# Optimization experiments

Hardware: AMD Instinct MI355X
Metric: run time of the kernel (lower is better)

Reference implementation:

```python
import jax, jax.numpy as jnp
import numpy as np

EPS = 10.0
MAX_ITER = 50
THRESH = 1e-05
N, M, D = 8192, 8192, 32


def setup_inputs() -> dict:
    key = jax.random.key(0)
    k1, k2, k3, k4 = jax.random.split(key, 4)
    x = jax.random.normal(k1, (N, D), dtype=jnp.float32)
    y = jax.random.normal(k2, (M, D), dtype=jnp.float32)
    p = jax.random.uniform(k3, (N,), dtype=jnp.float32)
    q = jax.random.uniform(k4, (M,), dtype=jnp.float32)
    p = p / jnp.sum(p)  # marginals must be probability vectors
    q = q / jnp.sum(q)
    return {"x": x, "y": y, "p": p, "q": q}


def _cost_matrix_l2(x, y):
    # ||x_i - y_j||^2 via the expansion, avoiding the [N, M, D] intermediate
    x2 = jnp.sum(x * x, axis=-1)  # [N]
    y2 = jnp.sum(y * y, axis=-1)  # [M]
    C = x2[:, None] + y2[None, :] - 2.0 * (x @ y.T)  # [N, M]
    return jnp.maximum(C, 0.0)


def reference(x, y, p, q):
    C = _cost_matrix_l2(x, y)          # [N, M]
    K = jnp.exp(-C / EPS)              # [N, M]

    def step(carry, _):
        a, b, done = carry
        a_new = p / (K @ b)            # [N]
        b_new = q / (K.T @ a_new)      # [M]
        err = jnp.linalg.norm(b_new - b)
        # emulate the early break: freeze (a, b) once err < thresh was hit
        a_out = jnp.where(done, a, a_new)
        b_out = jnp.where(done, b, b_new)
        done = jnp.logical_or(done, err < THRESH)
        return (a_out, b_out, done), None

    init = (jnp.zeros_like(p), jnp.ones_like(q), jnp.array(False))
    (a, b, _), _ = jax.lax.scan(step, init, None, length=MAX_ITER)

    T = a[:, None] * K * b[None, :]    # diag(a) @ K @ diag(b)
    w_cost = jnp.sum(T * C)
    return w_cost, T
```

## Files before the change

### kernel.cpp

```cpp
#include <hip/hip_runtime.h>
#include <hip/hip_fp16.h>


#define NN 8192
#define DDIM 32
#define EPSF 10.0f
#define LOG2E 1.44269504088896340736f
#define LN2F 0.69314718055994530942f
#define KLOG2 8.0f
#define THRESH2 1e-10f

#define OFF_KS   0ull
#define OFF_PART (67108864ull)
#define OFF_A    (OFF_PART + 8388608ull)
#define OFF_B    (OFF_A + 32768ull)
#define OFF_X2   (OFF_B + 32768ull)
#define OFF_Y2   (OFF_X2 + 32768ull)
#define OFF_ERR  (OFF_Y2 + 32768ull)
#define WS_NEEDED (OFF_ERR + 4096ull)

typedef float floatx2 __attribute__((ext_vector_type(2)));

#if __has_builtin(__builtin_amdgcn_cvt_pk_f32_fp8) && __has_builtin(__builtin_amdgcn_cvt_pk_fp8_f32)
#define HW_FP8 1
#else
#define HW_FP8 0
#include <hip/hip_fp8.h>
#endif

__device__ __forceinline__ void fp8x4_to_f32(unsigned int w, float* f) {
#if HW_FP8
    floatx2 lo = __builtin_amdgcn_cvt_pk_f32_fp8((int)w, false);
    floatx2 hi = __builtin_amdgcn_cvt_pk_f32_fp8((int)w, true);
    f[0] = lo.x; f[1] = lo.y; f[2] = hi.x; f[3] = hi.y;
#else
    for (int i = 0; i < 4; ++i) {
        __hip_fp8_e4m3 h; h.__x = (__hip_fp8_storage_t)((w >> (8 * i)) & 0xff);
        f[i] = (float)h;
    }
#endif
}

__device__ __forceinline__ unsigned char f32_to_fp8(float v) {
#if HW_FP8
    return (unsigned char)(__builtin_amdgcn_cvt_pk_fp8_f32(v, v, 0, false) & 0xff);
#else
    __hip_fp8_e4m3 h(v);
    return (unsigned char)h.__x;
#endif
}

__global__ __launch_bounds__(256) void k_init(const float* __restrict__ x,
                                              const float* __restrict__ y,
                                              float* __restrict__ x2,
                                              float* __restrict__ y2,
                                              float* __restrict__ b,
                                              float* __restrict__ errpart,
                                              float* __restrict__ out) {
    int t = blockIdx.x * 256 + threadIdx.x;
    const float4* x4 = (const float4*)(x + (size_t)t * DDIM);
    float s = 0.f;
#pragma unroll
    for (int k = 0; k < 8; ++k) { float4 v = x4[k]; s += v.x*v.x + v.y*v.y + v.z*v.z + v.w*v.w; }
    x2[t] = s;
    const float4* y4 = (const float4*)(y + (size_t)t * DDIM);
    s = 0.f;
#pragma unroll
    for (int k = 0; k < 8; ++k) { float4 v = y4[k]; s += v.x*v.x + v.y*v.y + v.z*v.z + v.w*v.w; }
    y2[t] = s;
    b[t] = 1.0f;
    if (t < 256) errpart[t] = 1e30f;
    if (t == 0) out[0] = 0.f;
}

__global__ __launch_bounds__(256) void k_build(const float* __restrict__ x,
                                               const float* __restrict__ y,
                                               const float* __restrict__ x2,
                                               const float* __restrict__ y2,
                                               unsigned char* __restrict__ Ks) {
    __shared__ float yT[DDIM][256];
    __shared__ float xT[DDIM][32];
    __shared__ __align__(16) unsigned char hb8[32][256];
    const int t = threadIdx.x;
    const int jb = blockIdx.x & 31;
    const int ib = blockIdx.x >> 5;
    const int colbase = jb * 256, rowbase = ib * 32;

    {
        const float4* yp = (const float4*)(y + (size_t)(colbase + t) * DDIM);
#pragma unroll
        for (int k = 0; k < 8; ++k) {
            float4 v = yp[k];
            yT[4*k+0][t] = v.x; yT[4*k+1][t] = v.y; yT[4*k+2][t] = v.z; yT[4*k+3][t] = v.w;
        }
    }
    {
        int r = t >> 3, ds = (t & 7) * 4;
        float4 v = *(const float4*)(x + (size_t)(rowbase + r) * DDIM + ds);
        xT[ds+0][r] = v.x; xT[ds+1][r] = v.y; xT[ds+2][r] = v.z; xT[ds+3][r] = v.w;
    }
    __syncthreads();

    float acc[32];
#pragma unroll
    for (int r = 0; r < 32; ++r) acc[r] = 0.f;
    for (int d = 0; d < DDIM; ++d) {
        float yv = yT[d][t];
#pragma unroll
        for (int r4 = 0; r4 < 8; ++r4) {
            float4 xv = *(const float4*)&xT[d][r4 * 4];
            acc[r4*4+0] = fmaf(xv.x, yv, acc[r4*4+0]);
            acc[r4*4+1] = fmaf(xv.y, yv, acc[r4*4+1]);
            acc[r4*4+2] = fmaf(xv.z, yv, acc[r4*4+2]);
            acc[r4*4+3] = fmaf(xv.w, yv, acc[r4*4+3]);
        }
    }
    const float y2c = y2[colbase + t];
#pragma unroll
    for (int r = 0; r < 32; ++r) {
        float Cv = fmaxf(x2[rowbase + r] + y2c - 2.f * acc[r], 0.f);
        float arg = KLOG2 - Cv * (LOG2E / EPSF);
        hb8[r][t] = f32_to_fp8(__builtin_amdgcn_exp2f(arg));
    }
    __syncthreads();
    {
        int row = t >> 3, off = (t & 7) * 32;
        uint4 v0 = *(const uint4*)&hb8[row][off];
        uint4 v1 = *(const uint4*)&hb8[row][off + 16];
        unsigned char* dst = Ks + (size_t)(rowbase + row) * NN + colbase + off;
        *(uint4*)dst = v0;
        *(uint4*)(dst + 16) = v1;
    }
}

#define ROWFMA(KV, KC) { \
    const unsigned int* kw_ = (const unsigned int*)&(KV); \
    _Pragma("unroll") \
    for (int j4 = 0; j4 < 4; ++j4) { \
        float kf_[4]; \
        fp8x4_to_f32(kw_[j4], kf_); \
        float4 bv_ = b4[((KC) * 4 + j4) * 64 + lane]; \
        rs = fmaf(kf_[0], bv_.x, rs); \
        rs = fmaf(kf_[1], bv_.y, rs); \
        rs = fmaf(kf_[2], bv_.z, rs); \
        rs = fmaf(kf_[3], bv_.w, rs); \
    } }

#define COLFMA(KV, AV) { \
    float kf_[8]; \
    fp8x4_to_f32((KV).x, kf_); \
    fp8x4_to_f32((KV).y, kf_ + 4); \
    _Pragma("unroll") \
    for (int j = 0; j < 8; ++j) cacc[j] = fmaf(kf_[j], (AV), cacc[j]); }

__global__ __launch_bounds__(1024) void k_iter(const unsigned char* __restrict__ Ks,
                                               const float* __restrict__ bg,
                                               const float* __restrict__ p,
                                               float* __restrict__ a_out,
                                               float* __restrict__ part,
                                               const float* __restrict__ errpart) {
    __shared__ float bsw[NN];
    __shared__ float rowhalf[2][8][2];
    __shared__ float dred[17];
    const int t = threadIdx.x;
    const int w = t >> 6, lane = t & 63;
    const int band = blockIdx.x * 32;
    const int rl = w >> 1, half = w & 1;

    float4 g0 = ((const float4*)bg)[2 * t];
    float4 g1 = ((const float4*)bg)[2 * t + 1];
    float e = (t < 256) ? errpart[t] : 0.f;
    const uint4* kp0 = (const uint4*)(Ks + (size_t)(band + rl) * NN + half * 4096);
    uint4 ka0 = kp0[lane], ka1 = kp0[64 + lane], ka2 = kp0[128 + lane], ka3 = kp0[192 + lane];
    __builtin_amdgcn_sched_barrier(0);

#pragma unroll
    for (int off = 32; off > 0; off >>= 1) e += __shfl_down(e, off, 64);
    if (lane == 0) dred[w] = e;
    __syncthreads();
    if (t == 0) dred[16] = (dred[0] + dred[1]) + (dred[2] + dred[3]);
    __syncthreads();
    if (dred[16] < THRESH2) return;

    {
        float vals[8] = {g0.x, g0.y, g0.z, g0.w, g1.x, g1.y, g1.z, g1.w};
        int c0 = t * 8;
#pragma unroll
        for (int u = 0; u < 8; ++u) {
            int c = c0 + u;
            bsw[(c >> 10) * 1024 + ((c >> 2) & 3) * 256 + ((c >> 4) & 63) * 4 + (c & 3)] = vals[u];
        }
    }
    __syncthreads();

    float cacc[8] = {0.f, 0.f, 0.f, 0.f, 0.f, 0.f, 0.f, 0.f};
    const float4* b4 = (const float4*)bsw;

#pragma unroll
    for (int sub = 0; sub < 4; ++sub) {
        const int sb = sub & 1;
        const uint2* kp2 = (const uint2*)(Ks + (size_t)(band + sub * 8) * NN);
        uint2 cv0 = kp2[0 * (NN / 8) + t], cv1 = kp2[1 * (NN / 8) + t],
              cv2 = kp2[2 * (NN / 8) + t], cv3 = kp2[3 * (NN / 8) + t],
              cv4 = kp2[4 * (NN / 8) + t], cv5 = kp2[5 * (NN / 8) + t],
              cv6 = kp2[6 * (NN / 8) + t], cv7 = kp2[7 * (NN / 8) + t];
        uint4 kb0 = {0,0,0,0}, kb1 = {0,0,0,0}, kb2 = {0,0,0,0}, kb3 = {0,0,0,0};
        if (sub < 3) {
            const uint4* kp = (const uint4*)(Ks + (size_t)(band + (sub + 1) * 8 + rl) * NN + half * 4096);
            kb0 = kp[lane]; kb1 = kp[64 + lane]; kb2 = kp[128 + lane]; kb3 = kp[192 + lane];
        }
        __builtin_amdgcn_sched_barrier(0);

        float rs = 0.f;
        ROWFMA(ka0, half * 4 + 0)
        ROWFMA(ka1, half * 4 + 1)
        ROWFMA(ka2, half * 4 + 2)
        ROWFMA(ka3, half * 4 + 3)
#pragma unroll
        for (int off = 32; off > 0; off >>= 1) rs += __shfl_down(rs, off, 64);
        if (lane == 0) rowhalf[sb][rl][half] = rs;
        __syncthreads();

        const int rg = band + sub * 8;
        float av0 = p[rg + 0] / (rowhalf[sb][0][0] + rowhalf[sb][0][1]);
        float av1 = p[rg + 1] / (rowhalf[sb][1][0] + rowhalf[sb][1][1]);
        float av2 = p[rg + 2] / (rowhalf[sb][2][0] + rowhalf[sb][2][1]);
        float av3 = p[rg + 3] / (rowhalf[sb][3][0] + rowhalf[sb][3][1]);
        float av4 = p[rg + 4] / (rowhalf[sb][4][0] + rowhalf[sb][4][1]);
        float av5 = p[rg + 5] / (rowhalf[sb][5][0] + rowhalf[sb][5][1]);
        float av6 = p[rg + 6] / (rowhalf[sb][6][0] + rowhalf[sb][6][1]);
        float av7 = p[rg + 7] / (rowhalf[sb][7][0] + rowhalf[sb][7][1]);
        if (t == 0) {
            *(float4*)(a_out + rg)     = make_float4(av0, av1, av2, av3);
            *(float4*)(a_out + rg + 4) = make_float4(av4, av5, av6, av7);
        }

        COLFMA(cv0, av0)
        COLFMA(cv1, av1)
        COLFMA(cv2, av2)
        COLFMA(cv3, av3)
        COLFMA(cv4, av4)
        COLFMA(cv5, av5)
        COLFMA(cv6, av6)
        COLFMA(cv7, av7)

        if (sub < 3) { ka0 = kb0; ka1 = kb1; ka2 = kb2; ka3 = kb3; }
    }
    float4* pp = (float4*)(part + (size_t)blockIdx.x * NN + t * 8);
    pp[0] = make_float4(cacc[0], cacc[1], cacc[2], cacc[3]);
    pp[1] = make_float4(cacc[4], cacc[5], cacc[6], cacc[7]);
}

__global__ __launch_bounds__(256) void k_div(const float* __restrict__ part,
                                             const float* __restrict__ q,
                                             float* __restrict__ b,
                                             float* __restrict__ errpart) {
    const int t = threadIdx.x;
    __shared__ float red[8][32];
    __shared__ float esc[32];
    __shared__ float dsum[5];
    {
        float e = errpart[t];
#pragma unroll
        for (int off = 32; off > 0; off >>= 1) e += __shfl_down(e, off, 64);
        if ((t & 63) == 0) dsum[t >> 6] = e;
        __syncthreads();
        if (t == 0) dsum[4] = (dsum[0] + dsum[1]) + (dsum[2] + dsum[3]);
        __syncthreads();
        if (dsum[4] < THRESH2) return;
    }
    const int c = t & 31, ibc = t >> 5;
    const int col = blockIdx.x * 32 + c;
    float s = 0.f;
#pragma unroll 4
    for (int i = 0; i < 32; ++i) s += part[(size_t)(ibc * 32 + i) * NN + col];
    red[ibc][c] = s;
    __syncthreads();
    if (ibc == 0) {
        float sum = 0.f;
#pragma unroll
        for (int k = 0; k < 8; ++k) sum += red[k][c];
        float bn = q[col] / sum;
        float d = bn - b[col];
        b[col] = bn;
        esc[c] = d * d;
    }
    __syncthreads();
    if (t == 0) {
        float e = 0.f;
#pragma unroll
        for (int k = 0; k < 32; ++k) e += esc[k];
        errpart[blockIdx.x] = e;
    }
}

__global__ __launch_bounds__(256) void k_final(const unsigned char* __restrict__ Ks,
                                               const float* __restrict__ a,
                                               const float* __restrict__ b,
                                               float* __restrict__ out) {
    const int t = threadIdx.x;
    const int row = blockIdx.x;
    const float ai = a[row];
    const uint2* kp = (const uint2*)(Ks + (size_t)row * NN);
    float* Trow = out + 1 + (size_t)row * NN;
    float w = 0.f;
    const float c1 = EPSF * LN2F;
#pragma unroll
    for (int k = 0; k < 4; ++k) {
        const int col = k * 2048 + t * 8;
        uint2 kv = kp[k * 256 + t];
        float kf[8];
        fp8x4_to_f32(kv.x, kf);
        fp8x4_to_f32(kv.y, kf + 4);
        float4 b0 = *(const float4*)(b + col);
        float4 b1 = *(const float4*)(b + col + 4);
        float bv[8] = {b0.x, b0.y, b0.z, b0.w, b1.x, b1.y, b1.z, b1.w};
#pragma unroll
        for (int j = 0; j < 8; ++j) {
            float ks = kf[j];
            float Tv = ai * ks * bv[j];
            float Cv = c1 * (KLOG2 - __builtin_amdgcn_logf(fmaxf(ks, 1e-35f)));
            w = fmaf(Tv, Cv, w);
            Trow[col + j] = Tv;
        }
    }
#pragma unroll
    for (int off = 32; off > 0; off >>= 1) w += __shfl_down(w, off, 64);
    __shared__ float red[4];
    if ((t & 63) == 0) red[t >> 6] = w;
    __syncthreads();
    if (t == 0) atomicAdd(out, (red[0] + red[1]) + (red[2] + red[3]));
}

extern "C" void kernel_launch(void* const* d_in, const int* in_sizes, int n_in,
                              void* d_out, int out_size, void* d_ws, size_t ws_size,
                              hipStream_t stream) {
    const float* x = (const float*)d_in[0];
    const float* y = (const float*)d_in[1];
    const float* p = (const float*)d_in[2];
    const float* q = (const float*)d_in[3];
    float* out = (float*)d_out;
    if (ws_size < WS_NEEDED) return;
    char* ws = (char*)d_ws;
    unsigned char* Ks = (unsigned char*)(ws + OFF_KS);
    float* part = (float*)(ws + OFF_PART);
    float* a = (float*)(ws + OFF_A);
    float* b = (float*)(ws + OFF_B);
    float* x2 = (float*)(ws + OFF_X2);
    float* y2 = (float*)(ws + OFF_Y2);
    float* errpart = (float*)(ws + OFF_ERR);

    k_init<<<dim3(32), dim3(256), 0, stream>>>(x, y, x2, y2, b, errpart, out);
    k_build<<<dim3(8192), dim3(256), 0, stream>>>(x, y, x2, y2, Ks);
    for (int it = 0; it < 50; ++it) {
        k_iter<<<dim3(256), dim3(1024), 0, stream>>>(Ks, b, p, a, part, errpart);
        k_div<<<dim3(256), dim3(256), 0, stream>>>(part, q, b, errpart);
    }
    k_final<<<dim3(8192), dim3(256), 0, stream>>>(Ks, a, b, out);
}
```

Measured before the change: 1.755 ms.

## Use atomic double-buffered error scalar and packed fp8 conversion with vector FMAs

The convergence error moves from a 256-entry partial array, reduced by every block of both kernels, to a single double-buffered scalar that k_div accumulates with atomics. Each block now reads one value instead of doing a shuffle and shared-memory reduction with two barriers. The inner row and column products use the hardware packed fp8-to-f32 conversion and two-wide float vectors so the compiler can emit packed FMAs, and the per-row division becomes a hardware reciprocal multiply. The trade-offs are nondeterministic atomic summation order and slightly lower reciprocal precision.

Result: slower. 1.792 ms (+2.2%).

```diff
diff --git a/kernel.cpp b/kernel.cpp
--- a/kernel.cpp
+++ b/kernel.cpp
@@ -55,7 +55,7 @@
                                               float* __restrict__ x2,
                                               float* __restrict__ y2,
                                               float* __restrict__ b,
-                                              float* __restrict__ errpart,
+                                              float* __restrict__ err,
                                               float* __restrict__ out) {
     int t = blockIdx.x * 256 + threadIdx.x;
     const float4* x4 = (const float4*)(x + (size_t)t * DDIM);
@@ -69,7 +69,7 @@
     for (int k = 0; k < 8; ++k) { float4 v = y4[k]; s += v.x*v.x + v.y*v.y + v.z*v.z + v.w*v.w; }
     y2[t] = s;
     b[t] = 1.0f;
-    if (t < 256) errpart[t] = 1e30f;
+    if (t < 2) err[t] = 1e30f;
     if (t == 0) out[0] = 0.f;
 }
 
@@ -133,6 +133,26 @@
     }
 }
 
+#if HW_FP8
+#define ROWFMA(KV, KC) { \
+    const unsigned int* kw_ = (const unsigned int*)&(KV); \
+    _Pragma("unroll") \
+    for (int j4 = 0; j4 < 4; ++j4) { \
+        floatx2 lo_ = __builtin_amdgcn_cvt_pk_f32_fp8((int)kw_[j4], false); \
+        floatx2 hi_ = __builtin_amdgcn_cvt_pk_f32_fp8((int)kw_[j4], true); \
+        const floatx2* bp_ = (const floatx2*)(b4 + ((KC) * 4 + j4) * 64 + lane); \
+        rs2a += lo_ * bp_[0]; \
+        rs2b += hi_ * bp_[1]; \
+    } }
+#define COLFMA(KV, AV) { \
+    floatx2 av2_; av2_.x = (AV); av2_.y = (AV); \
+    floatx2 l0_ = __builtin_amdgcn_cvt_pk_f32_fp8((int)(KV).x, false); \
+    floatx2 h0_ = __builtin_amdgcn_cvt_pk_f32_fp8((int)(KV).x, true); \
+    floatx2 l1_ = __builtin_amdgcn_cvt_pk_f32_fp8((int)(KV).y, false); \
+    floatx2 h1_ = __builtin_amdgcn_cvt_pk_f32_fp8((int)(KV).y, true); \
+    cacc2[0] += l0_ * av2_; cacc2[1] += h0_ * av2_; \
+    cacc2[2] += l1_ * av2_; cacc2[3] += h1_ * av2_; }
+#else
 #define ROWFMA(KV, KC) { \
     const unsigned int* kw_ = (const unsigned int*)&(KV); \
     _Pragma("unroll") \
@@ -140,28 +160,33 @@
         float kf_[4]; \
         fp8x4_to_f32(kw_[j4], kf_); \
         float4 bv_ = b4[((KC) * 4 + j4) * 64 + lane]; \
-        rs = fmaf(kf_[0], bv_.x, rs); \
-        rs = fmaf(kf_[1], bv_.y, rs); \
-        rs = fmaf(kf_[2], bv_.z, rs); \
-        rs = fmaf(kf_[3], bv_.w, rs); \
+        rs2a.x = fmaf(kf_[0], bv_.x, rs2a.x); \
+        rs2b.x = fmaf(kf_[1], bv_.y, rs2b.x); \
+        rs2a.y = fmaf(kf_[2], bv_.z, rs2a.y); \
+        rs2b.y = fmaf(kf_[3], bv_.w, rs2b.y); \
     } }
-
 #define COLFMA(KV, AV) { \
     float kf_[8]; \
     fp8x4_to_f32((KV).x, kf_); \
     fp8x4_to_f32((KV).y, kf_ + 4); \
-    _Pragma("unroll") \
-    for (int j = 0; j < 8; ++j) cacc[j] = fmaf(kf_[j], (AV), cacc[j]); }
+    cacc2[0].x = fmaf(kf_[0], (AV), cacc2[0].x); \
+    cacc2[0].y = fmaf(kf_[1], (AV), cacc2[0].y); \
+    cacc2[1].x = fmaf(kf_[2], (AV), cacc2[1].x); \
+    cacc2[1].y = fmaf(kf_[3], (AV), cacc2[1].y); \
+    cacc2[2].x = fmaf(kf_[4], (AV), cacc2[2].x); \
+    cacc2[2].y = fmaf(kf_[5], (AV), cacc2[2].y); \
+    cacc2[3].x = fmaf(kf_[6], (AV), cacc2[3].x); \
+    cacc2[3].y = fmaf(kf_[7], (AV), cacc2[3].y); }
+#endif
 
 __global__ __launch_bounds__(1024) void k_iter(const unsigned char* __restrict__ Ks,
                                                const float* __restrict__ bg,
                                                const float* __restrict__ p,
                                                float* __restrict__ a_out,
                                                float* __restrict__ part,
-                                               const float* __restrict__ errpart) {
+                                               float* __restrict__ err, int it) {
     __shared__ float bsw[NN];
     __shared__ float rowhalf[2][8][2];
-    __shared__ float dred[17];
     const int t = threadIdx.x;
     const int w = t >> 6, lane = t & 63;
     const int band = blockIdx.x * 32;
@@ -169,18 +194,12 @@
 
     float4 g0 = ((const float4*)bg)[2 * t];
     float4 g1 = ((const float4*)bg)[2 * t + 1];
-    float e = (t < 256) ? errpart[t] : 0.f;
     const uint4* kp0 = (const uint4*)(Ks + (size_t)(band + rl) * NN + half * 4096);
     uint4 ka0 = kp0[lane], ka1 = kp0[64 + lane], ka2 = kp0[128 + lane], ka3 = kp0[192 + lane];
+    float ev = err[(it ^ 1) & 1];
+    if (blockIdx.x == 0 && t == 0) err[it & 1] = 0.f;
     __builtin_amdgcn_sched_barrier(0);
-
-#pragma unroll
-    for (int off = 32; off > 0; off >>= 1) e += __shfl_down(e, off, 64);
-    if (lane == 0) dred[w] = e;
-    __syncthreads();
-    if (t == 0) dred[16] = (dred[0] + dred[1]) + (dred[2] + dred[3]);
-    __syncthreads();
-    if (dred[16] < THRESH2) return;
+    if (ev < THRESH2) return;
 
     {
         float vals[8] = {g0.x, g0.y, g0.z, g0.w, g1.x, g1.y, g1.z, g1.w};
@@ -193,7 +212,9 @@
     }
     __syncthreads();
 
-    float cacc[8] = {0.f, 0.f, 0.f, 0.f, 0.f, 0.f, 0.f, 0.f};
+    floatx2 cacc2[4];
+    cacc2[0] = floatx2{0.f, 0.f}; cacc2[1] = floatx2{0.f, 0.f};
+    cacc2[2] = floatx2{0.f, 0.f}; cacc2[3] = floatx2{0.f, 0.f};
     const float4* b4 = (const float4*)bsw;
 
 #pragma unroll
@@ -211,25 +232,26 @@
         }
         __builtin_amdgcn_sched_barrier(0);
 
-        float rs = 0.f;
+        floatx2 rs2a = floatx2{0.f, 0.f}, rs2b = floatx2{0.f, 0.f};
         ROWFMA(ka0, half * 4 + 0)
         ROWFMA(ka1, half * 4 + 1)
         ROWFMA(ka2, half * 4 + 2)
         ROWFMA(ka3, half * 4 + 3)
+        float rs = (rs2a.x + rs2a.y) + (rs2b.x + rs2b.y);
 #pragma unroll
         for (int off = 32; off > 0; off >>= 1) rs += __shfl_down(rs, off, 64);
         if (lane == 0) rowhalf[sb][rl][half] = rs;
         __syncthreads();
 
         const int rg = band + sub * 8;
-        float av0 = p[rg + 0] / (rowhalf[sb][0][0] + rowhalf[sb][0][1]);
-        float av1 = p[rg + 1] / (rowhalf[sb][1][0] + rowhalf[sb][1][1]);
-        float av2 = p[rg + 2] / (rowhalf[sb][2][0] + rowhalf[sb][2][1]);
-        float av3 = p[rg + 3] / (rowhalf[sb][3][0] + rowhalf[sb][3][1]);
-        float av4 = p[rg + 4] / (rowhalf[sb][4][0] + rowhalf[sb][4][1]);
-        float av5 = p[rg + 5] / (rowhalf[sb][5][0] + rowhalf[sb][5][1]);
-        float av6 = p[rg + 6] / (rowhalf[sb][6][0] + rowhalf[sb][6][1]);
-        float av7 = p[rg + 7] / (rowhalf[sb][7][0] + rowhalf[sb][7][1]);
+        float av0 = p[rg + 0] * __builtin_amdgcn_rcpf(rowhalf[sb][0][0] + rowhalf[sb][0][1]);
+        float av1 = p[rg + 1] * __builtin_amdgcn_rcpf(rowhalf[sb][1][0] + rowhalf[sb][1][1]);
+        float av2 = p[rg + 2] * __builtin_amdgcn_rcpf(rowhalf[sb][2][0] + rowhalf[sb][2][1]);
+        float av3 = p[rg + 3] * __builtin_amdgcn_rcpf(rowhalf[sb][3][0] + rowhalf[sb][3][1]);
+        float av4 = p[rg + 4] * __builtin_amdgcn_rcpf(rowhalf[sb][4][0] + rowhalf[sb][4][1]);
+        float av5 = p[rg + 5] * __builtin_amdgcn_rcpf(rowhalf[sb][5][0] + rowhalf[sb][5][1]);
+        float av6 = p[rg + 6] * __builtin_amdgcn_rcpf(rowhalf[sb][6][0] + rowhalf[sb][6][1]);
+        float av7 = p[rg + 7] * __builtin_amdgcn_rcpf(rowhalf[sb][7][0] + rowhalf[sb][7][1]);
         if (t == 0) {
             *(float4*)(a_out + rg)     = make_float4(av0, av1, av2, av3);
             *(float4*)(a_out + rg + 4) = make_float4(av4, av5, av6, av7);
@@ -247,33 +269,23 @@
         if (sub < 3) { ka0 = kb0; ka1 = kb1; ka2 = kb2; ka3 = kb3; }
     }
     float4* pp = (float4*)(part + (size_t)blockIdx.x * NN + t * 8);
-    pp[0] = make_float4(cacc[0], cacc[1], cacc[2], cacc[3]);
-    pp[1] = make_float4(cacc[4], cacc[5], cacc[6], cacc[7]);
+    pp[0] = make_float4(cacc2[0].x, cacc2[0].y, cacc2[1].x, cacc2[1].y);
+    pp[1] = make_float4(cacc2[2].x, cacc2[2].y, cacc2[3].x, cacc2[3].y);
 }
 
 __global__ __launch_bounds__(256) void k_div(const float* __restrict__ part,
                                              const float* __restrict__ q,
                                              float* __restrict__ b,
-                                             float* __restrict__ errpart) {
+                                             float* __restrict__ err, int it) {
+    if (err[(it ^ 1) & 1] < THRESH2) return;
     const int t = threadIdx.x;
-    __shared__ float red[8][32];
-    __shared__ float esc[32];
-    __shared__ float dsum[5];
-    {
-        float e = errpart[t];
-#pragma unroll
-        for (int off = 32; off > 0; off >>= 1) e += __shfl_down(e, off, 64);
-        if ((t & 63) == 0) dsum[t >> 6] = e;
-        __syncthreads();
-        if (t == 0) dsum[4] = (dsum[0] + dsum[1]) + (dsum[2] + dsum[3]);
-        __syncthreads();
-        if (dsum[4] < THRESH2) return;
-    }
     const int c = t & 31, ibc = t >> 5;
     const int col = blockIdx.x * 32 + c;
     float s = 0.f;
 #pragma unroll 4
     for (int i = 0; i < 32; ++i) s += part[(size_t)(ibc * 32 + i) * NN + col];
+    __shared__ float red[8][32];
+    __shared__ float esc[32];
     red[ibc][c] = s;
     __syncthreads();
     if (ibc == 0) {
@@ -290,7 +302,7 @@
         float e = 0.f;
 #pragma unroll
         for (int k = 0; k < 32; ++k) e += esc[k];
-        errpart[blockIdx.x] = e;
+        atomicAdd(&err[it & 1], e);
     }
 }
 
@@ -348,13 +360,13 @@
     float* b = (float*)(ws + OFF_B);
     float* x2 = (float*)(ws + OFF_X2);
     float* y2 = (float*)(ws + OFF_Y2);
-    float* errpart = (float*)(ws + OFF_ERR);
-
-    k_init<<<dim3(32), dim3(256), 0, stream>>>(x, y, x2, y2, b, errpart, out);
+    float* err = (float*)(ws + OFF_ERR);
+
+    k_init<<<dim3(32), dim3(256), 0, stream>>>(x, y, x2, y2, b, err, out);
     k_build<<<dim3(8192), dim3(256), 0, stream>>>(x, y, x2, y2, Ks);
     for (int it = 0; it < 50; ++it) {
-        k_iter<<<dim3(256), dim3(1024), 0, stream>>>(Ks, b, p, a, part, errpart);
-        k_div<<<dim3(256), dim3(256), 0, stream>>>(part, q, b, errpart);
+        k_iter<<<dim3(256), dim3(1024), 0, stream>>>(Ks, b, p, a, part, err, it);
+        k_div<<<dim3(256), dim3(256), 0, stream>>>(part, q, b, err, it);
     }
     k_final<<<dim3(8192), dim3(256), 0, stream>>>(Ks, a, b, out);
 }
```
